# Optimization experiments

Hardware: AMD Instinct MI355X
Metric: run time of the kernel (lower is better)

The kernel has to match this reference:

```python
import jax, jax.numpy as jnp
import numpy as np


def _cdist(p1, p2):
    # Euclidean cdist via the matmul expansion (matches torch.cdist p=2 fast path):
    # ||a-b||^2 = ||a||^2 + ||b||^2 - 2 a.b ; clamp tiny negatives before sqrt.
    sq1 = jnp.sum(p1 * p1, axis=-1, keepdims=True)        # (N, 1)
    sq2 = jnp.sum(p2 * p2, axis=-1, keepdims=True).T      # (1, M)
    d2 = sq1 + sq2 - 2.0 * (p1 @ p2.T)                    # (N, M)
    return jnp.sqrt(jnp.maximum(d2, 0.0))


def setup_inputs() -> dict:
    key = jax.random.key(0)
    k1, k2 = jax.random.split(key)
    N, M = 16384, 16384
    points1 = jax.random.normal(k1, (N, 3), dtype=jnp.float32)
    points2 = jax.random.normal(k2, (M, 3), dtype=jnp.float32)
    return {"points1": points1, "points2": points2}


def reference(points1, points2):
    dist = _cdist(points1, points2)                        # (N, M)
    min1 = jnp.min(dist, axis=1)                           # (N,) nearest in points2
    min2 = jnp.min(dist, axis=0)                           # (M,) nearest in points1
    return jnp.sum(min1) + jnp.sum(min2)
```

## Files before the change

kernel.cpp:

```cpp
#include <hip/hip_runtime.h>
#include <hip/hip_bf16.h>
#include <math.h>


typedef _Float16 half8    __attribute__((ext_vector_type(8)));
typedef float    floatx16 __attribute__((ext_vector_type(16)));

constexpr int CH   = 2048;
constexpr int ROWS = 128;
constexpr int BLK  = 256;

__global__ __launch_bounds__(BLK, 4) void chamfer_sweep_kernel(
    const float* __restrict__ P1, const float* __restrict__ P2,
    float* __restrict__ part, float* __restrict__ out,
    int n1, int n2, int YC)
{
    __shared__ uint2 sB[CH];
    __shared__ float sRowMin[ROWS];

    const int dir  = blockIdx.z;
    const float* A = dir == 0 ? P1 : P2;
    const float* B = dir == 0 ? P2 : P1;
    const int nA   = dir == 0 ? n1 : n2;
    const int nB   = dir == 0 ? n2 : n1;
    float* pbase   = part + (dir == 0 ? 0 : (size_t)YC * n1);

    const int tid  = threadIdx.x;
    const int wave = tid >> 6;
    const int lane = tid & 63;
    const int n    = lane & 31;
    const int g    = lane >> 5;
    const bool g0  = (g == 0);

    if (blockIdx.x == 0 && blockIdx.y == 0 && blockIdx.z == 0 && tid == 0)
        out[0] = 0.0f;

    const int bstart = blockIdx.y * CH;
    for (int i = tid; i < CH; i += BLK) {
        int j = bstart + i; if (j >= nB) j = nB - 1;
        float bx = B[3*j], by = B[3*j+1], bz = B[3*j+2];
        _Float16 hx = (_Float16)bx, hy = (_Float16)by, hz = (_Float16)bz;
        float qx = (float)hx, qy = (float)hy, qz = (float)hz;
        _Float16 hw = (_Float16)(qx*qx + qy*qy + qz*qz);
        union { _Float16 h[4]; uint2 u; } p;
        p.h[0] = hx; p.h[1] = hy; p.h[2] = hz; p.h[3] = hw;
        sB[i] = p.u;
    }

    const _Float16 h0 = (_Float16)0.0f;
    half8 af;
    {
        int row = blockIdx.x * ROWS + wave * 32 + n;
        if (row >= nA) row = nA - 1;
        float ax = A[3*row], ay = A[3*row+1], az = A[3*row+2];
        _Float16 hax = (_Float16)ax, hay = (_Float16)ay, haz = (_Float16)az;
        float qx = (float)hax, qy = (float)hay, qz = (float)haz;
        _Float16 hs = (_Float16)(qx*qx + qy*qy + qz*qz);
        af[0] = g0 ? (_Float16)(-2.0f * qx) : h0;
        af[1] = g0 ? (_Float16)(-2.0f * qy) : h0;
        af[2] = g0 ? (_Float16)(-2.0f * qz) : h0;
        af[3] = g0 ? (_Float16)1.0f : h0;
        af[4] = g0 ? hs : h0;
        af[5] = h0; af[6] = h0; af[7] = h0;
    }

    __syncthreads();

    floatx16 rowmin;
#pragma unroll
    for (int r = 0; r < 16; ++r) rowmin[r] = 1e30f;
    const floatx16 zacc = {};

    union BF { half8 v; unsigned u[4]; uint2 lo; };
    BF bu0, bu1, bu2, bu3;
    { union { _Float16 h[2]; unsigned u; } q;
      q.h[0] = (_Float16)1.0f; q.h[1] = h0;
      bu0.u[2] = q.u; bu0.u[3] = 0u;
      bu1.u[2] = q.u; bu1.u[3] = 0u;
      bu2.u[2] = q.u; bu2.u[3] = 0u;
      bu3.u[2] = q.u; bu3.u[3] = 0u; }

    for (int bt = 0; bt < CH / 128; ++bt) {
        const uint2* p = sB + bt * 128 + n;
        bu0.lo = p[0];
        bu1.lo = p[32];
        bu2.lo = p[64];
        bu3.lo = p[96];

        floatx16 d0 = __builtin_amdgcn_mfma_f32_32x32x16_f16(af, bu0.v, zacc, 0, 0, 0);
        floatx16 d1 = __builtin_amdgcn_mfma_f32_32x32x16_f16(af, bu1.v, zacc, 0, 0, 0);
        floatx16 d2 = __builtin_amdgcn_mfma_f32_32x32x16_f16(af, bu2.v, zacc, 0, 0, 0);
        floatx16 d3 = __builtin_amdgcn_mfma_f32_32x32x16_f16(af, bu3.v, zacc, 0, 0, 0);

#pragma unroll
        for (int r = 0; r < 16; ++r) {
            float t = fminf(fminf(rowmin[r], d0[r]), d1[r]);
            rowmin[r] = fminf(fminf(t, d2[r]), d3[r]);
        }
    }

#pragma unroll
    for (int mask = 1; mask <= 16; mask <<= 1)
#pragma unroll
        for (int r = 0; r < 16; ++r)
            rowmin[r] = fminf(rowmin[r], __shfl_xor(rowmin[r], mask));

    if (n == 0) {
#pragma unroll
        for (int r = 0; r < 16; ++r) {
            int rr = wave * 32 + g * 4 + ((r & 3) + 8 * (r >> 2));
            sRowMin[rr] = rowmin[r];
        }
    }
    __syncthreads();

    if (tid < ROWS) {
        int grow = blockIdx.x * ROWS + tid;
        if (grow < nA) pbase[(size_t)grow * YC + blockIdx.y] = sRowMin[tid];
    }
}

__global__ __launch_bounds__(256) void reduce_kernel(
    const float* __restrict__ part, float* __restrict__ out,
    int ntot, int YC)
{
    __shared__ float s[256];
    int r = blockIdx.x * 256 + threadIdx.x;
    float acc = 0.0f;
    if (r < ntot) {
        const float* p = part + (size_t)r * YC;
        float m = 1e30f;
        for (int y = 0; y < YC; ++y) m = fminf(m, p[y]);
        acc = sqrtf(fmaxf(m, 0.0f));
    }
    s[threadIdx.x] = acc;
    __syncthreads();
    for (int w = 128; w > 0; w >>= 1) {
        if (threadIdx.x < w) s[threadIdx.x] += s[threadIdx.x + w];
        __syncthreads();
    }
    if (threadIdx.x == 0) atomicAdd(out, s[0]);
}

extern "C" void kernel_launch(void* const* d_in, const int* in_sizes, int n_in,
                              void* d_out, int out_size, void* d_ws, size_t ws_size,
                              hipStream_t stream) {
    const float* P1 = (const float*)d_in[0];
    const float* P2 = (const float*)d_in[1];
    const int n1 = in_sizes[0] / 3;
    const int n2 = in_sizes[1] / 3;
    const int nmax = (n1 > n2) ? n1 : n2;
    const int YC = (nmax + CH - 1) / CH;

    float* part = (float*)d_ws;
    float* out  = (float*)d_out;

    {
        dim3 grid((nmax + ROWS - 1) / ROWS, YC, 2);
        chamfer_sweep_kernel<<<grid, BLK, 0, stream>>>(P1, P2, part, out, n1, n2, YC);
    }
    int nb = (n1 + n2 + 255) / 256;
    reduce_kernel<<<nb, 256, 0, stream>>>(part, out, n1 + n2, YC);
}
```

Baseline: 79.84 us.

## Pre-pack points to fp16 in a separate kernel, double chunk size

Adds a pack kernel that converts each point set once to packed fp16 (x,y,z,|p|^2) records in workspace. The sweep kernel then bulk-copies these records into shared memory with 16-byte loads instead of converting strided fp32 data in every block. CH doubles to 4096, so there are fewer y-chunks and fewer partial minima, and the reduce kernel gains a float4 fast path for YC==4. The cost is an extra kernel launch and more workspace, plus fewer blocks and more shared memory per block, which may reduce occupancy.

```diff
diff --git a/kernel.cpp b/kernel.cpp
--- a/kernel.cpp
+++ b/kernel.cpp
@@ -6,24 +6,43 @@
 typedef _Float16 half8    __attribute__((ext_vector_type(8)));
 typedef float    floatx16 __attribute__((ext_vector_type(16)));
 
-constexpr int CH   = 2048;
+constexpr int CH   = 4096;
 constexpr int ROWS = 128;
 constexpr int BLK  = 256;
 
+__global__ __launch_bounds__(256) void pack_kernel(
+    const float* __restrict__ P1, const float* __restrict__ P2,
+    uint2* __restrict__ F1, uint2* __restrict__ F2,
+    int n1, int n2, int NP, float* __restrict__ out)
+{
+    int i = blockIdx.x * 256 + threadIdx.x;
+    if (i == 0) out[0] = 0.0f;
+    const float* P; uint2* F; int n, idx;
+    if (i < NP)          { P = P1; F = F1; n = n1; idx = i; }
+    else if (i < 2 * NP) { P = P2; F = F2; n = n2; idx = i - NP; }
+    else return;
+    int j = idx < n ? idx : n - 1;
+    float x = P[3*j], y = P[3*j+1], z = P[3*j+2];
+    _Float16 hx = (_Float16)x, hy = (_Float16)y, hz = (_Float16)z;
+    float qx = (float)hx, qy = (float)hy, qz = (float)hz;
+    _Float16 hw = (_Float16)(qx*qx + qy*qy + qz*qz);
+    union { _Float16 h[4]; uint2 u; } p;
+    p.h[0] = hx; p.h[1] = hy; p.h[2] = hz; p.h[3] = hw;
+    F[idx] = p.u;
+}
+
 __global__ __launch_bounds__(BLK, 4) void chamfer_sweep_kernel(
-    const float* __restrict__ P1, const float* __restrict__ P2,
-    float* __restrict__ part, float* __restrict__ out,
-    int n1, int n2, int YC)
+    const uint2* __restrict__ F1, const uint2* __restrict__ F2,
+    float* __restrict__ part, int n1, int n2, int YC)
 {
     __shared__ uint2 sB[CH];
     __shared__ float sRowMin[ROWS];
 
-    const int dir  = blockIdx.z;
-    const float* A = dir == 0 ? P1 : P2;
-    const float* B = dir == 0 ? P2 : P1;
-    const int nA   = dir == 0 ? n1 : n2;
-    const int nB   = dir == 0 ? n2 : n1;
-    float* pbase   = part + (dir == 0 ? 0 : (size_t)YC * n1);
+    const int dir   = blockIdx.z;
+    const uint2* FA = dir == 0 ? F1 : F2;
+    const uint2* FB = dir == 0 ? F2 : F1;
+    const int nA    = dir == 0 ? n1 : n2;
+    float* pbase    = part + (dir == 0 ? 0 : (size_t)YC * n1);
 
     const int tid  = threadIdx.x;
     const int wave = tid >> 6;
@@ -32,35 +51,23 @@
     const int g    = lane >> 5;
     const bool g0  = (g == 0);
 
-    if (blockIdx.x == 0 && blockIdx.y == 0 && blockIdx.z == 0 && tid == 0)
-        out[0] = 0.0f;
-
-    const int bstart = blockIdx.y * CH;
-    for (int i = tid; i < CH; i += BLK) {
-        int j = bstart + i; if (j >= nB) j = nB - 1;
-        float bx = B[3*j], by = B[3*j+1], bz = B[3*j+2];
-        _Float16 hx = (_Float16)bx, hy = (_Float16)by, hz = (_Float16)bz;
-        float qx = (float)hx, qy = (float)hy, qz = (float)hz;
-        _Float16 hw = (_Float16)(qx*qx + qy*qy + qz*qz);
-        union { _Float16 h[4]; uint2 u; } p;
-        p.h[0] = hx; p.h[1] = hy; p.h[2] = hz; p.h[3] = hw;
-        sB[i] = p.u;
+    {
+        const uint4* src = (const uint4*)(FB + (size_t)blockIdx.y * CH);
+        uint4* dst = (uint4*)sB;
+        for (int i = tid; i < CH / 2; i += BLK) dst[i] = src[i];
     }
 
     const _Float16 h0 = (_Float16)0.0f;
     half8 af;
     {
-        int row = blockIdx.x * ROWS + wave * 32 + n;
-        if (row >= nA) row = nA - 1;
-        float ax = A[3*row], ay = A[3*row+1], az = A[3*row+2];
-        _Float16 hax = (_Float16)ax, hay = (_Float16)ay, haz = (_Float16)az;
-        float qx = (float)hax, qy = (float)hay, qz = (float)haz;
-        _Float16 hs = (_Float16)(qx*qx + qy*qy + qz*qz);
-        af[0] = g0 ? (_Float16)(-2.0f * qx) : h0;
-        af[1] = g0 ? (_Float16)(-2.0f * qy) : h0;
-        af[2] = g0 ? (_Float16)(-2.0f * qz) : h0;
+        int arow = blockIdx.x * ROWS + wave * 32 + n;
+        union { uint2 u; _Float16 h[4]; } au; au.u = FA[arow];
+        const _Float16 m2 = (_Float16)(-2.0f);
+        af[0] = g0 ? (_Float16)(au.h[0] * m2) : h0;
+        af[1] = g0 ? (_Float16)(au.h[1] * m2) : h0;
+        af[2] = g0 ? (_Float16)(au.h[2] * m2) : h0;
         af[3] = g0 ? (_Float16)1.0f : h0;
-        af[4] = g0 ? hs : h0;
+        af[4] = g0 ? au.h[3] : h0;
         af[5] = h0; af[6] = h0; af[7] = h0;
     }
 
@@ -128,9 +135,15 @@
     int r = blockIdx.x * 256 + threadIdx.x;
     float acc = 0.0f;
     if (r < ntot) {
-        const float* p = part + (size_t)r * YC;
-        float m = 1e30f;
-        for (int y = 0; y < YC; ++y) m = fminf(m, p[y]);
+        float m;
+        if (YC == 4) {
+            const float4 v = ((const float4*)part)[r];
+            m = fminf(fminf(v.x, v.y), fminf(v.z, v.w));
+        } else {
+            const float* p = part + (size_t)r * YC;
+            m = 1e30f;
+            for (int y = 0; y < YC; ++y) m = fminf(m, p[y]);
+        }
         acc = sqrtf(fmaxf(m, 0.0f));
     }
     s[threadIdx.x] = acc;
@@ -151,14 +164,18 @@
     const int n2 = in_sizes[1] / 3;
     const int nmax = (n1 > n2) ? n1 : n2;
     const int YC = (nmax + CH - 1) / CH;
+    const int NP = YC * CH;
 
-    float* part = (float*)d_ws;
+    uint2* F1   = (uint2*)d_ws;
+    uint2* F2   = F1 + NP;
+    float* part = (float*)(F2 + NP);
     float* out  = (float*)d_out;
 
+    pack_kernel<<<(2 * NP + 255) / 256, 256, 0, stream>>>(P1, P2, F1, F2, n1, n2, NP, out);
+
     {
-        dim3 grid((nmax + ROWS - 1) / ROWS, YC, 2);
-        chamfer_sweep_kernel<<<grid, BLK, 0, stream>>>(P1, P2, part, out, n1, n2, YC);
+        dim3 grid(NP / ROWS, YC, 2);
+        chamfer_sweep_kernel<<<grid, BLK, 0, stream>>>(F1, F2, part, n1, n2, YC);
     }
-    int nb = (n1 + n2 + 255) / 256;
-    reduce_kernel<<<nb, 256, 0, stream>>>(part, out, n1 + n2, YC);
+    reduce_kernel<<<(n1 + n2 + 255) / 256, 256, 0, stream>>>(part, out, n1 + n2, YC);
 }
```

After: 77.40 us. 3.0% less time.
